# Optimization experiments

Measured on AMD Instinct MI355X. Metric: run time of the kernel, lower is better.

The kernel has to match this reference:

```python
import jax, jax.numpy as jnp
import numpy as np

T, N, F_IN = 5, 10000, 16
E = 160000
C = 32          # gat_hidden_dim (per head)
H0 = 2          # heads in layer 0 (concat) -> out 64
GRU = 64
OUT_H = 32


def setup_inputs() -> dict:
    key = jax.random.key(0)
    ks = jax.random.split(key, 24)
    s = 0.1
    inp = {
        "x_seq": jax.random.normal(ks[0], (T, N, F_IN), jnp.float32),
        "edge_index": jax.random.randint(ks[1], (2, E), 0, N, jnp.int32),
        # GAT layer 0: in 16 -> 2 heads x 32, concat -> 64
        "gat0_W": s * jax.random.normal(ks[2], (F_IN, H0 * C), jnp.float32),
        "gat0_asrc": s * jax.random.normal(ks[3], (H0, C), jnp.float32),
        "gat0_adst": s * jax.random.normal(ks[4], (H0, C), jnp.float32),
        "gat0_b": s * jax.random.normal(ks[5], (H0 * C,), jnp.float32),
        "res0_W": s * jax.random.normal(ks[6], (F_IN, H0 * C), jnp.float32),   # [in,out]
        # GAT layer 1: in 64 -> 1 head x 32, no concat -> 32
        "gat1_W": s * jax.random.normal(ks[7], (H0 * C, C), jnp.float32),
        "gat1_asrc": s * jax.random.normal(ks[8], (1, C), jnp.float32),
        "gat1_adst": s * jax.random.normal(ks[9], (1, C), jnp.float32),
        "gat1_b": s * jax.random.normal(ks[10], (C,), jnp.float32),
        "res1_W": s * jax.random.normal(ks[11], (H0 * C, C), jnp.float32),
        # GRU cells (torch GRUCell layout: W_i [3H,in], W_h [3H,H])
        "gru0_Wi": s * jax.random.normal(ks[12], (3 * GRU, C), jnp.float32),
        "gru0_Wh": s * jax.random.normal(ks[13], (3 * GRU, GRU), jnp.float32),
        "gru0_bi": s * jax.random.normal(ks[14], (3 * GRU,), jnp.float32),
        "gru0_bh": s * jax.random.normal(ks[15], (3 * GRU,), jnp.float32),
        "gru1_Wi": s * jax.random.normal(ks[16], (3 * GRU, GRU), jnp.float32),
        "gru1_Wh": s * jax.random.normal(ks[17], (3 * GRU, GRU), jnp.float32),
        "gru1_bi": s * jax.random.normal(ks[18], (3 * GRU,), jnp.float32),
        "gru1_bh": s * jax.random.normal(ks[19], (3 * GRU,), jnp.float32),
        # MLP head
        "fc1_W": s * jax.random.normal(ks[20], (GRU, OUT_H), jnp.float32),
        "fc1_b": s * jax.random.normal(ks[21], (OUT_H,), jnp.float32),
        "fc2_W": s * jax.random.normal(ks[22], (OUT_H, 1), jnp.float32),
        "fc2_b": s * jax.random.normal(ks[23], (1,), jnp.float32),
    }
    return inp


def _gat(x, src, dst, n, W, a_src, a_dst, b, heads, concat):
    ch = W.shape[1] // heads
    xw = (x @ W).reshape(n, heads, ch)                      # [N,H,C]
    al_s = (xw * a_src).sum(-1)                             # [N,H]
    al_d = (xw * a_dst).sum(-1)
    e = jax.nn.leaky_relu(al_s[src] + al_d[dst], 0.2)       # [Etot,H]
    m = jax.ops.segment_max(e, dst, num_segments=n)
    ex = jnp.exp(e - m[dst])
    den = jax.ops.segment_sum(ex, dst, num_segments=n)
    alpha = ex / (den[dst] + 1e-16)                         # scatter-softmax
    out = jax.ops.segment_sum(alpha[:, :, None] * xw[src], dst, num_segments=n)
    out = out.reshape(n, heads * ch) if concat else out.mean(axis=1)
    return out + b


def _gru(x, h, Wi, Wh, bi, bh):
    gi = x @ Wi.T + bi
    gh = h @ Wh.T + bh
    i_r, i_z, i_n = jnp.split(gi, 3, axis=-1)
    h_r, h_z, h_n = jnp.split(gh, 3, axis=-1)
    r = jax.nn.sigmoid(i_r + h_r)
    z = jax.nn.sigmoid(i_z + h_z)
    nn_ = jnp.tanh(i_n + r * h_n)
    return (1.0 - z) * nn_ + z * h


def reference(x_seq, edge_index,
              gat0_W, gat0_asrc, gat0_adst, gat0_b, res0_W,
              gat1_W, gat1_asrc, gat1_adst, gat1_b, res1_W,
              gru0_Wi, gru0_Wh, gru0_bi, gru0_bh,
              gru1_Wi, gru1_Wh, gru1_bi, gru1_bh,
              fc1_W, fc1_b, fc2_W, fc2_b):
    n = x_seq.shape[1]
    loops = jnp.arange(n, dtype=edge_index.dtype)
    src = jnp.concatenate([edge_index[0], loops])           # PyG adds self-loops
    dst = jnp.concatenate([edge_index[1], loops])

    def step(carry, x_t):
        h0, h1 = carry
        x1 = jax.nn.elu(_gat(x_t, src, dst, n, gat0_W, gat0_asrc, gat0_adst, gat0_b, 2, True)) + x_t @ res0_W
        x2 = jax.nn.elu(_gat(x1, src, dst, n, gat1_W, gat1_asrc, gat1_adst, gat1_b, 1, False)) + x1 @ res1_W
        h0 = _gru(x2, h0, gru0_Wi, gru0_Wh, gru0_bi, gru0_bh)
        h1 = _gru(h0, h1, gru1_Wi, gru1_Wh, gru1_bi, gru1_bh)
        return (h0, h1), None

    h0 = jnp.zeros((n, gru0_Wh.shape[1]), x_seq.dtype)
    h1 = jnp.zeros((n, gru1_Wh.shape[1]), x_seq.dtype)
    (h0, h1), _ = jax.lax.scan(step, (h0, h1), x_seq)
    h = jax.nn.relu(h1 @ fc1_W + fc1_b)
    return h @ fc2_W + fc2_b                                # [N,1]
```

## Files before the change

### kernel.cpp

```cpp
#include <hip/hip_runtime.h>
#include <hip/hip_bf16.h>
#include <math.h>

#define T_STEPS 5
#define NNODES  10000
#define NM      (T_STEPS * NNODES)
#define F_IN    16
#define NEDGES  160000
#define ETOT    (NEDGES + NNODES)
#define GNPW    4

#define RL(v, k) __int_as_float(__builtin_amdgcn_readlane(__float_as_int(v), (k)))

__global__ __launch_bounds__(256) void k_count(const int* __restrict__ ei, int* __restrict__ counts) {
    int idx = blockIdx.x * 256 + threadIdx.x;
    if (idx >= ETOT) return;
    int dst = (idx < NEDGES) ? ei[NEDGES + idx] : (idx - NEDGES);
    atomicAdd(&counts[dst], 1);
}

__global__ __launch_bounds__(1024) void k_scan(const int* __restrict__ counts, int* __restrict__ offs) {
    __shared__ int ssum[1024];
    int t = threadIdx.x;
    const int chunk = (NNODES + 1023) / 1024;
    int start = t * chunk, end = min(start + chunk, NNODES);
    int s = 0;
    for (int i = start; i < end; i++) s += counts[i];
    ssum[t] = s;
    __syncthreads();
    for (int off = 1; off < 1024; off <<= 1) {
        int v = (t >= off) ? ssum[t - off] : 0;
        __syncthreads();
        ssum[t] += v;
        __syncthreads();
    }
    int excl = (t == 0) ? 0 : ssum[t - 1];
    for (int i = start; i < end; i++) { offs[i] = excl; excl += counts[i]; }
    if (t == 1023) offs[NNODES] = ssum[1023];
}

__global__ __launch_bounds__(256) void k_fill(const int* __restrict__ ei, const int* __restrict__ offs,
                                              int* __restrict__ cursor, int* __restrict__ csr) {
    int idx = blockIdx.x * 256 + threadIdx.x;
    if (idx >= ETOT) return;
    int src, dst;
    if (idx < NEDGES) { src = ei[idx]; dst = ei[NEDGES + idx]; }
    else              { src = dst = idx - NEDGES; }
    int p = atomicAdd(&cursor[dst], 1);
    csr[offs[dst] + p] = src;
}

__global__ __launch_bounds__(256) void k_transpose(const float* __restrict__ Wi0, const float* __restrict__ Wh0,
                                                   const float* __restrict__ Wi1, const float* __restrict__ Wh1,
                                                   float* __restrict__ WiT0, float* __restrict__ WhT0,
                                                   float* __restrict__ WiT1, float* __restrict__ WhT1) {
    int idx = blockIdx.x * 256 + threadIdx.x;
    if (idx < 32 * 192) {
        int k = idx / 192, r = idx % 192;
        WiT0[idx] = Wi0[r * 32 + k];
        return;
    }
    idx -= 32 * 192;
    if (idx < 64 * 192) {
        int k = idx / 192, r = idx % 192;
        WhT0[idx] = Wh0[r * 64 + k];
        return;
    }
    idx -= 64 * 192;
    if (idx < 64 * 192) {
        int k = idx / 192, r = idx % 192;
        WiT1[idx] = Wi1[r * 64 + k];
        return;
    }
    idx -= 64 * 192;
    if (idx < 64 * 192) {
        int k = idx / 192, r = idx % 192;
        WhT1[idx] = Wh1[r * 64 + k];
    }
}

__global__ __launch_bounds__(256) void k_mm0_all(const float* __restrict__ x,
                                                 const float* __restrict__ W,
                                                 const float* __restrict__ Wres,
                                                 const float* __restrict__ asrc,
                                                 const float* __restrict__ adst,
                                                 float* __restrict__ xw, float* __restrict__ xres,
                                                 float* __restrict__ als, float* __restrict__ ald) {
    int wave = threadIdx.x >> 6, lane = threadIdx.x & 63;
    int m = blockIdx.x * 4 + wave;
    if (m >= NM) return;
    const float* xr = x + (size_t)m * F_IN;
    float xreg[F_IN];
#pragma unroll
    for (int k = 0; k < F_IN; k++) xreg[k] = xr[k];
    float acc = 0.f, accr = 0.f;
#pragma unroll
    for (int k = 0; k < F_IN; k++) {
        acc  += xreg[k] * W[k * 64 + lane];
        accr += xreg[k] * Wres[k * 64 + lane];
    }
    xw[(size_t)m * 64 + lane]   = acc;
    xres[(size_t)m * 64 + lane] = accr;
    float ps = acc * asrc[lane], pd = acc * adst[lane];
    for (int off = 16; off; off >>= 1) {
        ps += __shfl_down(ps, off, 32);
        pd += __shfl_down(pd, off, 32);
    }
    if ((lane & 31) == 0) {
        int h = lane >> 5;
        als[m * 2 + h] = ps;
        ald[m * 2 + h] = pd;
    }
}

__global__ __launch_bounds__(256) void k_gat0_all(const float* __restrict__ xw,
                                                  const float* __restrict__ xres,
                                                  const float* __restrict__ als,
                                                  const float* __restrict__ ald,
                                                  const int* __restrict__ offs, const int* __restrict__ csr,
                                                  const float* __restrict__ b,
                                                  const float* __restrict__ W1,
                                                  const float* __restrict__ Wres1,
                                                  const float* __restrict__ as1,
                                                  const float* __restrict__ ad1v,
                                                  float* __restrict__ xw1, float* __restrict__ xres1,
                                                  float* __restrict__ als1, float* __restrict__ ald1) {
    int wave = threadIdx.x >> 6, lane = threadIdx.x & 63;
    int m = blockIdx.x * 4 + wave;
    if (m >= NM) return;
    int t = m / NNODES;
    int node = m - t * NNODES;
    int base = t * NNODES;
    int beg = offs[node], end = offs[node + 1];
    int deg = end - beg;
    float ad0 = ald[m * 2 + 0], ad1 = ald[m * 2 + 1];
    float acc;
    if (deg <= 64) {
        int s = 0; float e0 = -INFINITY, e1 = -INFINITY;
        if (lane < deg) {
            s = base + csr[beg + lane];
            e0 = als[s * 2 + 0] + ad0; e0 = e0 > 0.f ? e0 : 0.2f * e0;
            e1 = als[s * 2 + 1] + ad1; e1 = e1 > 0.f ? e1 : 0.2f * e1;
        }
        float m0 = e0, m1 = e1;
        for (int o = 32; o; o >>= 1) {
            m0 = fmaxf(m0, __shfl_xor(m0, o));
            m1 = fmaxf(m1, __shfl_xor(m1, o));
        }
        float ex0 = (lane < deg) ? expf(e0 - m0) : 0.f;
        float ex1 = (lane < deg) ? expf(e1 - m1) : 0.f;
        float d0 = ex0, d1 = ex1;
        for (int o = 32; o; o >>= 1) {
            d0 += __shfl_xor(d0, o);
            d1 += __shfl_xor(d1, o);
        }
        ex0 *= 1.f / (d0 + 1e-16f);
        ex1 *= 1.f / (d1 + 1e-16f);
        float a0 = 0.f, a1 = 0.f, a2 = 0.f, a3 = 0.f;
        int i = 0;
        for (; i + 4 <= deg; i += 4) {
            int   s0 = __shfl(s, i),     s1 = __shfl(s, i + 1), s2 = __shfl(s, i + 2), s3 = __shfl(s, i + 3);
            float u0 = __shfl(ex0, i),   v0 = __shfl(ex1, i);
            float u1 = __shfl(ex0, i+1), v1 = __shfl(ex1, i+1);
            float u2 = __shfl(ex0, i+2), v2 = __shfl(ex1, i+2);
            float u3 = __shfl(ex0, i+3), v3 = __shfl(ex1, i+3);
            a0 += (lane < 32 ? u0 : v0) * xw[(size_t)s0 * 64 + lane];
            a1 += (lane < 32 ? u1 : v1) * xw[(size_t)s1 * 64 + lane];
            a2 += (lane < 32 ? u2 : v2) * xw[(size_t)s2 * 64 + lane];
            a3 += (lane < 32 ? u3 : v3) * xw[(size_t)s3 * 64 + lane];
        }
        for (; i < deg; i++) {
            int s0 = __shfl(s, i);
            float u = __shfl(ex0, i), v = __shfl(ex1, i);
            a0 += (lane < 32 ? u : v) * xw[(size_t)s0 * 64 + lane];
        }
        acc = (a0 + a1) + (a2 + a3);
    } else {
        float m0 = -INFINITY, m1 = -INFINITY;
        for (int i = beg + lane; i < end; i += 64) {
            int s = base + csr[i];
            float e0 = als[s * 2 + 0] + ad0; e0 = e0 > 0.f ? e0 : 0.2f * e0;
            float e1 = als[s * 2 + 1] + ad1; e1 = e1 > 0.f ? e1 : 0.2f * e1;
            m0 = fmaxf(m0, e0); m1 = fmaxf(m1, e1);
        }
        for (int o = 32; o; o >>= 1) {
            m0 = fmaxf(m0, __shfl_xor(m0, o));
            m1 = fmaxf(m1, __shfl_xor(m1, o));
        }
        float d0 = 0.f, d1 = 0.f;
        for (int i = beg + lane; i < end; i += 64) {
            int s = base + csr[i];
            float e0 = als[s * 2 + 0] + ad0; e0 = e0 > 0.f ? e0 : 0.2f * e0;
            float e1 = als[s * 2 + 1] + ad1; e1 = e1 > 0.f ? e1 : 0.2f * e1;
            d0 += expf(e0 - m0); d1 += expf(e1 - m1);
        }
        for (int o = 32; o; o >>= 1) { d0 += __shfl_xor(d0, o); d1 += __shfl_xor(d1, o); }
        float inv0 = 1.f / (d0 + 1e-16f), inv1 = 1.f / (d1 + 1e-16f);
        acc = 0.f;
        for (int i = beg; i < end; i++) {
            int s = base + csr[i];
            float e, wgt;
            if (lane < 32) { e = als[s * 2 + 0] + ad0; e = e > 0.f ? e : 0.2f * e; wgt = expf(e - m0) * inv0; }
            else           { e = als[s * 2 + 1] + ad1; e = e > 0.f ? e : 0.2f * e; wgt = expf(e - m1) * inv1; }
            acc += wgt * xw[(size_t)s * 64 + lane];
        }
    }
    float x1v = acc + b[lane];
    x1v = x1v > 0.f ? x1v : expm1f(x1v);
    x1v += xres[(size_t)m * 64 + lane];
    int j = lane & 31;
    const float* Wp = (lane < 32) ? W1 : Wres1;
    float pacc = 0.f;
#pragma unroll
    for (int k = 0; k < 64; k++) {
        float xv = RL(x1v, k);
        pacc += xv * Wp[k * 32 + j];
    }
    if (lane < 32) xw1[(size_t)m * 32 + j]   = pacc;
    else           xres1[(size_t)m * 32 + j] = pacc;
    float ps = (lane < 32) ? pacc * as1[j]  : 0.f;
    float pd = (lane < 32) ? pacc * ad1v[j] : 0.f;
    for (int o = 16; o; o >>= 1) {
        ps += __shfl_down(ps, o, 32);
        pd += __shfl_down(pd, o, 32);
    }
    if (lane == 0) { als1[m] = ps; ald1[m] = pd; }
}

__global__ __launch_bounds__(256) void k_gat1_all(const float* __restrict__ xw1,
                                                  const float* __restrict__ xres1,
                                                  const float* __restrict__ als1,
                                                  const float* __restrict__ ald1,
                                                  const int* __restrict__ offs, const int* __restrict__ csr,
                                                  const float* __restrict__ b,
                                                  float* __restrict__ x2) {
    int wave = threadIdx.x >> 6, lane = threadIdx.x & 63;
    int m = blockIdx.x * 4 + wave;
    if (m >= NM) return;
    int t = m / NNODES;
    int node = m - t * NNODES;
    int base = t * NNODES;
    int beg = offs[node], end = offs[node + 1];
    int deg = end - beg;
    float adv = ald1[m];
    int ch = lane & 31, half = lane >> 5;
    float aggr;
    if (deg <= 64) {
        int s = 0; float e = -INFINITY;
        if (lane < deg) {
            s = base + csr[beg + lane];
            e = als1[s] + adv; e = e > 0.f ? e : 0.2f * e;
        }
        float mx = e;
        for (int o = 32; o; o >>= 1) mx = fmaxf(mx, __shfl_xor(mx, o));
        float ex = (lane < deg) ? expf(e - mx) : 0.f;
        float d = ex;
        for (int o = 32; o; o >>= 1) d += __shfl_xor(d, o);
        ex *= 1.f / (d + 1e-16f);
        float acc = 0.f;
        for (int i = 0; i < deg; i += 2) {
            int i2 = (i + 1 < deg) ? i + 1 : i;
            int   sa = __shfl(s, i),  sb = __shfl(s, i2);
            float wa = __shfl(ex, i), wb = __shfl(ex, i2);
            if (i + 1 >= deg) wb = 0.f;
            int   sm = half ? sb : sa;
            float wm = half ? wb : wa;
            acc += wm * xw1[(size_t)sm * 32 + ch];
        }
        acc += __shfl_xor(acc, 32);
        aggr = acc;
    } else {
        float mx = -INFINITY;
        for (int i = beg + lane; i < end; i += 64) {
            float e = als1[base + csr[i]] + adv; e = e > 0.f ? e : 0.2f * e;
            mx = fmaxf(mx, e);
        }
        for (int o = 32; o; o >>= 1) mx = fmaxf(mx, __shfl_xor(mx, o));
        float d = 0.f;
        for (int i = beg + lane; i < end; i += 64) {
            float e = als1[base + csr[i]] + adv; e = e > 0.f ? e : 0.2f * e;
            d += expf(e - mx);
        }
        for (int o = 32; o; o >>= 1) d += __shfl_xor(d, o);
        float inv = 1.f / (d + 1e-16f);
        float acc = 0.f;
        for (int i = beg; i < end; i++) {
            int s = base + csr[i];
            float e = als1[s] + adv; e = e > 0.f ? e : 0.2f * e;
            float wgt = expf(e - mx) * inv;
            acc += wgt * xw1[(size_t)s * 32 + ch];
        }
        aggr = acc;
    }
    if (lane < 32) {
        float v = aggr + b[ch];
        v = v > 0.f ? v : expm1f(v);
        x2[(size_t)m * 32 + ch] = v + xres1[(size_t)m * 32 + ch];
    }
}

__global__ __launch_bounds__(256) void k_gruhead(const float* __restrict__ x2,
                                                 const float* __restrict__ WiT0,
                                                 const float* __restrict__ WhT0,
                                                 const float* __restrict__ WiT1,
                                                 const float* __restrict__ WhT1,
                                                 const float* __restrict__ bi0, const float* __restrict__ bh0,
                                                 const float* __restrict__ bi1, const float* __restrict__ bh1,
                                                 const float* __restrict__ fc1W,
                                                 const float* __restrict__ fc1b,
                                                 const float* __restrict__ fc2W,
                                                 const float* __restrict__ fc2b,
                                                 float* __restrict__ out) {
    int wave = threadIdx.x >> 6, lane = threadIdx.x & 63;
    int node0 = (blockIdx.x * 4 + wave) * GNPW;

    float bir0 = bi0[lane] + bh0[lane];
    float biz0 = bi0[64 + lane] + bh0[64 + lane];
    float bin0 = bi0[128 + lane], bhn0 = bh0[128 + lane];
    float bir1 = bi1[lane] + bh1[lane];
    float biz1 = bi1[64 + lane] + bh1[64 + lane];
    float bin1 = bi1[128 + lane], bhn1 = bh1[128 + lane];

    float h0[GNPW] = {0.f, 0.f, 0.f, 0.f};
    float h1[GNPW] = {0.f, 0.f, 0.f, 0.f};

    for (int t = 0; t < T_STEPS; t++) {
        float xa = x2[((size_t)t * NNODES + node0) * 32 + lane];
        float xb = x2[((size_t)t * NNODES + node0) * 32 + 64 + lane];

        float gr[GNPW], gz[GNPW], gin[GNPW], ghn[GNPW];
#pragma unroll
        for (int n = 0; n < GNPW; n++) { gr[n] = bir0; gz[n] = biz0; gin[n] = bin0; ghn[n] = bhn0; }
#pragma unroll 8
        for (int k = 0; k < 32; k++) {
            float wr = WiT0[k * 192 + lane];
            float wz = WiT0[k * 192 + 64 + lane];
            float wn = WiT0[k * 192 + 128 + lane];
            float xv[GNPW];
            xv[0] = RL(xa, k); xv[1] = RL(xa, 32 + k);
            xv[2] = RL(xb, k); xv[3] = RL(xb, 32 + k);
#pragma unroll
            for (int n = 0; n < GNPW; n++) {
                gr[n] += xv[n] * wr; gz[n] += xv[n] * wz; gin[n] += xv[n] * wn;
            }
        }
#pragma unroll 4
        for (int k = 0; k < 64; k++) {
            float wr = WhT0[k * 192 + lane];
            float wz = WhT0[k * 192 + 64 + lane];
            float wn = WhT0[k * 192 + 128 + lane];
#pragma unroll
            for (int n = 0; n < GNPW; n++) {
                float hv = RL(h0[n], k);
                gr[n] += hv * wr; gz[n] += hv * wz; ghn[n] += hv * wn;
            }
        }
#pragma unroll
        for (int n = 0; n < GNPW; n++) {
            float r = 1.f / (1.f + expf(-gr[n]));
            float z = 1.f / (1.f + expf(-gz[n]));
            float nn = tanhf(gin[n] + r * ghn[n]);
            h0[n] = (1.f - z) * nn + z * h0[n];
        }

#pragma unroll
        for (int n = 0; n < GNPW; n++) { gr[n] = bir1; gz[n] = biz1; gin[n] = bin1; ghn[n] = bhn1; }
#pragma unroll 4
        for (int k = 0; k < 64; k++) {
            float wir = WiT1[k * 192 + lane];
            float wiz = WiT1[k * 192 + 64 + lane];
            float win = WiT1[k * 192 + 128 + lane];
            float whr = WhT1[k * 192 + lane];
            float whz = WhT1[k * 192 + 64 + lane];
            float whn = WhT1[k * 192 + 128 + lane];
#pragma unroll
            for (int n = 0; n < GNPW; n++) {
                float xv = RL(h0[n], k);
                float hv = RL(h1[n], k);
                gr[n] += xv * wir + hv * whr;
                gz[n] += xv * wiz + hv * whz;
                gin[n] += xv * win;
                ghn[n] += hv * whn;
            }
        }
#pragma unroll
        for (int n = 0; n < GNPW; n++) {
            float r = 1.f / (1.f + expf(-gr[n]));
            float z = 1.f / (1.f + expf(-gz[n]));
            float nn = tanhf(gin[n] + r * ghn[n]);
            h1[n] = (1.f - z) * nn + z * h1[n];
        }
    }

    int j = lane & 31, half = lane >> 5;
#pragma unroll
    for (int p = 0; p < 2; p++) {
        float a = fc1b[j];
#pragma unroll
        for (int k = 0; k < 64; k++) {
            float he = RL(h1[2 * p], k);
            float ho = RL(h1[2 * p + 1], k);
            a += (half ? ho : he) * fc1W[k * 32 + j];
        }
        a = fmaxf(a, 0.f);
        float v = a * fc2W[j];
        for (int o = 16; o; o >>= 1) v += __shfl_down(v, o, 32);
        if ((lane & 31) == 0) out[node0 + 2 * p + half] = v + fc2b[0];
    }
}

extern "C" void kernel_launch(void* const* d_in, const int* in_sizes, int n_in,
                              void* d_out, int out_size, void* d_ws, size_t ws_size,
                              hipStream_t stream) {
    const float* x_seq   = (const float*)d_in[0];
    const int*   ei      = (const int*)d_in[1];
    const float* gat0_W  = (const float*)d_in[2];
    const float* gat0_as = (const float*)d_in[3];
    const float* gat0_ad = (const float*)d_in[4];
    const float* gat0_b  = (const float*)d_in[5];
    const float* res0_W  = (const float*)d_in[6];
    const float* gat1_W  = (const float*)d_in[7];
    const float* gat1_as = (const float*)d_in[8];
    const float* gat1_ad = (const float*)d_in[9];
    const float* gat1_b  = (const float*)d_in[10];
    const float* res1_W  = (const float*)d_in[11];
    const float* gru0_Wi = (const float*)d_in[12];
    const float* gru0_Wh = (const float*)d_in[13];
    const float* gru0_bi = (const float*)d_in[14];
    const float* gru0_bh = (const float*)d_in[15];
    const float* gru1_Wi = (const float*)d_in[16];
    const float* gru1_Wh = (const float*)d_in[17];
    const float* gru1_bi = (const float*)d_in[18];
    const float* gru1_bh = (const float*)d_in[19];
    const float* fc1_W   = (const float*)d_in[20];
    const float* fc1_b   = (const float*)d_in[21];
    const float* fc2_W   = (const float*)d_in[22];
    const float* fc2_b   = (const float*)d_in[23];
    float* out = (float*)d_out;

    char* w = (char*)d_ws;
    size_t off = 0;
    auto take = [&](size_t bytes) { size_t r = off; off += (bytes + 255) & ~(size_t)255; return r; };
    const size_t N = NNODES, M = NM;
    int*   counts = (int*)(w + take(N * 4));
    int*   cursor = (int*)(w + take(N * 4));
    int*   offs   = (int*)(w + take((N + 1) * 4));
    int*   csr    = (int*)(w + take((size_t)ETOT * 4));
    float* xw0    = (float*)(w + take(M * 64 * 4));
    float* xres0  = (float*)(w + take(M * 64 * 4));
    float* als0   = (float*)(w + take(M * 2 * 4));
    float* ald0   = (float*)(w + take(M * 2 * 4));
    float* xw1    = (float*)(w + take(M * 32 * 4));
    float* xres1  = (float*)(w + take(M * 32 * 4));
    float* als1   = (float*)(w + take(M * 4));
    float* ald1   = (float*)(w + take(M * 4));
    float* x2     = (float*)(w + take(M * 32 * 4));
    float* wiT0   = (float*)(w + take(32 * 192 * 4));
    float* whT0   = (float*)(w + take(64 * 192 * 4));
    float* wiT1   = (float*)(w + take(64 * 192 * 4));
    float* whT1   = (float*)(w + take(64 * 192 * 4));

    hipMemsetAsync(counts, 0, N * 4, stream);
    hipMemsetAsync(cursor, 0, N * 4, stream);
    const int egrid = (ETOT + 255) / 256;
    k_count<<<egrid, 256, 0, stream>>>(ei, counts);
    k_scan<<<1, 1024, 0, stream>>>(counts, offs);
    k_fill<<<egrid, 256, 0, stream>>>(ei, offs, cursor, csr);
    const int ttot = 32 * 192 + 3 * 64 * 192;
    k_transpose<<<(ttot + 255) / 256, 256, 0, stream>>>(gru0_Wi, gru0_Wh, gru1_Wi, gru1_Wh,
                                                        wiT0, whT0, wiT1, whT1);

    const int mgrid = (NM + 3) / 4;
    k_mm0_all<<<mgrid, 256, 0, stream>>>(x_seq, gat0_W, res0_W, gat0_as, gat0_ad, xw0, xres0, als0, ald0);
    k_gat0_all<<<mgrid, 256, 0, stream>>>(xw0, xres0, als0, ald0, offs, csr, gat0_b,
                                          gat1_W, res1_W, gat1_as, gat1_ad,
                                          xw1, xres1, als1, ald1);
    k_gat1_all<<<mgrid, 256, 0, stream>>>(xw1, xres1, als1, ald1, offs, csr, gat1_b, x2);

    const int ggrid = NNODES / (4 * GNPW);
    k_gruhead<<<ggrid, 256, 0, stream>>>(x2, wiT0, whT0, wiT1, whT1,
                                         gru0_bi, gru0_bh, gru1_bi, gru1_bh,
                                         fc1_W, fc1_b, fc2_W, fc2_b, out);
}
```

Measured before the change: 417.5 us.

## Stage GRU weight matrices in shared memory and widen GRU blocks

Measured after the change: 382.2 us. -8.5%, faster.

```diff
diff --git a/kernel.cpp b/kernel.cpp
--- a/kernel.cpp
+++ b/kernel.cpp
@@ -8,7 +8,8 @@
 #define F_IN    16
 #define NEDGES  160000
 #define ETOT    (NEDGES + NNODES)
-#define GNPW    4
+#define GW      8
+#define GNPW    5
 
 #define RL(v, k) __int_as_float(__builtin_amdgcn_readlane(__float_as_int(v), (k)))
 
@@ -299,7 +300,7 @@
     }
 }
 
-__global__ __launch_bounds__(256) void k_gruhead(const float* __restrict__ x2,
+__global__ __launch_bounds__(512) void k_gruhead(const float* __restrict__ x2,
                                                  const float* __restrict__ WiT0,
                                                  const float* __restrict__ WhT0,
                                                  const float* __restrict__ WiT1,
@@ -311,8 +312,10 @@
                                                  const float* __restrict__ fc2W,
                                                  const float* __restrict__ fc2b,
                                                  float* __restrict__ out) {
-    int wave = threadIdx.x >> 6, lane = threadIdx.x & 63;
-    int node0 = (blockIdx.x * 4 + wave) * GNPW;
+    __shared__ float lw[64 * 192];
+    int tid = threadIdx.x;
+    int wave = tid >> 6, lane = tid & 63;
+    int node0 = (blockIdx.x * GW + wave) * GNPW;
 
     float bir0 = bi0[lane] + bh0[lane];
     float biz0 = bi0[64 + lane] + bh0[64 + lane];
@@ -321,17 +324,28 @@
     float biz1 = bi1[64 + lane] + bh1[64 + lane];
     float bin1 = bi1[128 + lane], bhn1 = bh1[128 + lane];
 
-    float h0[GNPW] = {0.f, 0.f, 0.f, 0.f};
-    float h1[GNPW] = {0.f, 0.f, 0.f, 0.f};
+    float h0[GNPW] = {0.f, 0.f, 0.f, 0.f, 0.f};
+    float h1[GNPW] = {0.f, 0.f, 0.f, 0.f, 0.f};
+
+    auto stage = [&](const float* __restrict__ src) {
+        __syncthreads();
+        const float4* s4 = (const float4*)src;
+        float4* d4 = (float4*)lw;
+#pragma unroll
+        for (int i = 0; i < 6; i++) d4[tid + i * 512] = s4[tid + i * 512];
+        __syncthreads();
+    };
 
     for (int t = 0; t < T_STEPS; t++) {
-        float xa = x2[((size_t)t * NNODES + node0) * 32 + lane];
-        float xb = x2[((size_t)t * NNODES + node0) * 32 + 64 + lane];
+        size_t rb = ((size_t)t * NNODES + node0) * 32;
+        float xa = x2[rb + lane];
+        float xb = x2[rb + 64 + lane];
+        float xc = x2[rb + 128 + (lane & 31)];
 
         float gr[GNPW], gz[GNPW], gin[GNPW], ghn[GNPW];
 #pragma unroll
         for (int n = 0; n < GNPW; n++) { gr[n] = bir0; gz[n] = biz0; gin[n] = bin0; ghn[n] = bhn0; }
-#pragma unroll 8
+#pragma unroll 4
         for (int k = 0; k < 32; k++) {
             float wr = WiT0[k * 192 + lane];
             float wz = WiT0[k * 192 + 64 + lane];
@@ -339,16 +353,18 @@
             float xv[GNPW];
             xv[0] = RL(xa, k); xv[1] = RL(xa, 32 + k);
             xv[2] = RL(xb, k); xv[3] = RL(xb, 32 + k);
+            xv[4] = RL(xc, k);
 #pragma unroll
             for (int n = 0; n < GNPW; n++) {
                 gr[n] += xv[n] * wr; gz[n] += xv[n] * wz; gin[n] += xv[n] * wn;
             }
         }
+        stage(WhT0);
 #pragma unroll 4
         for (int k = 0; k < 64; k++) {
-            float wr = WhT0[k * 192 + lane];
-            float wz = WhT0[k * 192 + 64 + lane];
-            float wn = WhT0[k * 192 + 128 + lane];
+            float wr = lw[k * 192 + lane];
+            float wz = lw[k * 192 + 64 + lane];
+            float wn = lw[k * 192 + 128 + lane];
 #pragma unroll
             for (int n = 0; n < GNPW; n++) {
                 float hv = RL(h0[n], k);
@@ -364,23 +380,31 @@
         }
 
 #pragma unroll
-        for (int n = 0; n < GNPW; n++) { gr[n] = bir1; gz[n] = biz1; gin[n] = bin1; ghn[n] = bhn1; }
+        for (int n = 0; n < GNPW; n++) { gr[n] = bir1; gz[n] = biz1; gin[n] = bin1; }
+        stage(WiT1);
 #pragma unroll 4
         for (int k = 0; k < 64; k++) {
-            float wir = WiT1[k * 192 + lane];
-            float wiz = WiT1[k * 192 + 64 + lane];
-            float win = WiT1[k * 192 + 128 + lane];
-            float whr = WhT1[k * 192 + lane];
-            float whz = WhT1[k * 192 + 64 + lane];
-            float whn = WhT1[k * 192 + 128 + lane];
+            float wir = lw[k * 192 + lane];
+            float wiz = lw[k * 192 + 64 + lane];
+            float win = lw[k * 192 + 128 + lane];
 #pragma unroll
             for (int n = 0; n < GNPW; n++) {
                 float xv = RL(h0[n], k);
+                gr[n] += xv * wir; gz[n] += xv * wiz; gin[n] += xv * win;
+            }
+        }
+#pragma unroll
+        for (int n = 0; n < GNPW; n++) ghn[n] = bhn1;
+        stage(WhT1);
+#pragma unroll 4
+        for (int k = 0; k < 64; k++) {
+            float whr = lw[k * 192 + lane];
+            float whz = lw[k * 192 + 64 + lane];
+            float whn = lw[k * 192 + 128 + lane];
+#pragma unroll
+            for (int n = 0; n < GNPW; n++) {
                 float hv = RL(h1[n], k);
-                gr[n] += xv * wir + hv * whr;
-                gz[n] += xv * wiz + hv * whz;
-                gin[n] += xv * win;
-                ghn[n] += hv * whn;
+                gr[n] += hv * whr; gz[n] += hv * whz; ghn[n] += hv * whn;
             }
         }
 #pragma unroll
@@ -394,18 +418,20 @@
 
     int j = lane & 31, half = lane >> 5;
 #pragma unroll
-    for (int p = 0; p < 2; p++) {
+    for (int p = 0; p < 3; p++) {
+        int ne = 2 * p;
+        int no = (2 * p + 1 < GNPW) ? 2 * p + 1 : 2 * p;
         float a = fc1b[j];
 #pragma unroll
         for (int k = 0; k < 64; k++) {
-            float he = RL(h1[2 * p], k);
-            float ho = RL(h1[2 * p + 1], k);
+            float he = RL(h1[ne], k);
+            float ho = RL(h1[no], k);
             a += (half ? ho : he) * fc1W[k * 32 + j];
         }
         a = fmaxf(a, 0.f);
         float v = a * fc2W[j];
         for (int o = 16; o; o >>= 1) v += __shfl_down(v, o, 32);
-        if ((lane & 31) == 0) out[node0 + 2 * p + half] = v + fc2b[0];
+        if ((lane & 31) == 0 && 2 * p + half < GNPW) out[node0 + 2 * p + half] = v + fc2b[0];
     }
 }
 
@@ -477,8 +503,8 @@
                                           xw1, xres1, als1, ald1);
     k_gat1_all<<<mgrid, 256, 0, stream>>>(xw1, xres1, als1, ald1, offs, csr, gat1_b, x2);
 
-    const int ggrid = NNODES / (4 * GNPW);
-    k_gruhead<<<ggrid, 256, 0, stream>>>(x2, wiT0, whT0, wiT1, whT1,
+    const int ggrid = NNODES / (GW * GNPW);
+    k_gruhead<<<ggrid, 512, 0, stream>>>(x2, wiT0, whT0, wiT1, whT1,
                                          gru0_bi, gru0_bh, gru1_bi, gru1_bh,
                                          fc1_W, fc1_b, fc2_W, fc2_b, out);
 }
```
